# Performance work log

Hardware: AMD Instinct MI355X
Metric: run time of the kernel (lower is better)

## Reference

```python
import jax, jax.numpy as jnp
import numpy as np

K = 9  # ATSS top-k candidates per GT


def cxcywh_to_xyxy(b):
    cx, cy, w, h = b[..., 0], b[..., 1], b[..., 2], b[..., 3]
    return jnp.stack([cx - 0.5 * w, cy - 0.5 * h, cx + 0.5 * w, cy + 0.5 * h], axis=-1)


def elementwise_iou(a, b):
    # a, b: [..., 4] xyxy, broadcastable
    lt = jnp.maximum(a[..., :2], b[..., :2])
    rb = jnp.minimum(a[..., 2:], b[..., 2:])
    wh = jnp.clip(rb - lt, 0.0)
    inter = wh[..., 0] * wh[..., 1]
    area_a = (a[..., 2] - a[..., 0]) * (a[..., 3] - a[..., 1])
    area_b = (b[..., 2] - b[..., 0]) * (b[..., 3] - b[..., 1])
    return inter / (area_a + area_b - inter)


def setup_inputs() -> dict:
    key = jax.random.key(0)
    k1, k2 = jax.random.split(key)
    pred_boxes = jax.random.uniform(k1, (16, 30000, 4), dtype=jnp.float32)
    gt_boxes = jax.random.uniform(k2, (16, 64, 4), dtype=jnp.float32)
    return {"pred_boxes": pred_boxes, "gt_boxes": gt_boxes}


def reference(pred_boxes, gt_boxes):
    # pred_boxes: [B, N, 4] cxcywh; gt_boxes: [B, G, 4] cxcywh
    G = gt_boxes.shape[1]

    def per_image(pred, gt):
        # center-distance matrix [G, N] (the cdist in the original)
        diff = gt[:, None, :2] - pred[None, :, :2]
        dist = jnp.sqrt(jnp.sum(diff * diff, axis=-1))
        # k smallest distances per GT
        _, k_idx = jax.lax.top_k(-dist, K)          # [G, K]
        k_boxes = pred[k_idx]                        # [G, K, 4]
        gt_xyxy = cxcywh_to_xyxy(gt)                 # [G, 4]
        kb_xyxy = cxcywh_to_xyxy(k_boxes)            # [G, K, 4]
        ious = elementwise_iou(gt_xyxy[:, None, :], kb_xyxy)  # [G, K]
        # adaptive threshold: mean + std (torch.std is unbiased -> ddof=1)
        thr = jnp.mean(ious, axis=1, keepdims=True) + jnp.std(ious, axis=1, ddof=1, keepdims=True)
        cx, cy = k_boxes[..., 0], k_boxes[..., 1]
        inside = ((gt_xyxy[:, None, 0] <= cx) & (cx <= gt_xyxy[:, None, 2]) &
                  (gt_xyxy[:, None, 1] <= cy) & (cy <= gt_xyxy[:, None, 3]))
        mask = (ious >= thr) & inside                # [G, K]
        # padded index representation (original returns ragged lists):
        pred_idx = jnp.where(mask, k_idx, -1)
        gt_idx = jnp.where(mask, jnp.arange(G, dtype=jnp.int64)[:, None], -1)
        return pred_idx, gt_idx, mask, ious

    return jax.vmap(per_image)(pred_boxes, gt_boxes)
```

## Files before the change

kernel.cpp:

```cpp
#include <hip/hip_runtime.h>
#include <stdint.h>

typedef unsigned long long u64;

#define KCAND 9
#define BATCH 16
#define NPRED 30000
#define NGT   64
#define TPB   256
#define UNR   8
#define PPT   (TPB * UNR)
#define NT    15
#define PSTR  (NT * PPT)
#define INITKEY 0x7F800000FFFFFFFFULL
#define FINF  __uint_as_float(0x7F800000u)

__device__ __forceinline__ u64 wave_min_u64(u64 v) {
#pragma unroll
    for (int s = 1; s < 64; s <<= 1) {
        u64 o = __shfl_xor(v, s, 64);
        v = o < v ? o : v;
    }
    return v;
}

__global__ __launch_bounds__(256) void compact_xy(
    const float* __restrict__ pred, float2* __restrict__ xy)
{
    int e = blockIdx.x * 256 + threadIdx.x;
    int b = e / PSTR;
    int i = e - b * PSTR;
    float2 v;
    if (i < NPRED) {
        float4 p = ((const float4*)pred)[(size_t)b * NPRED + i];
        v = make_float2(p.x, p.y);
    } else {
        v = make_float2(FINF, FINF);
    }
    xy[e] = v;
}

template <bool PADDED>
__global__ __launch_bounds__(TPB, 4) void atss_kernel(
    const float2* __restrict__ xy,
    const float*  __restrict__ pred,
    const float*  __restrict__ gt,
    float* __restrict__ out)
{
#pragma clang fp contract(off)
    const int tid  = threadIdx.x;
    const int lane = tid & 63;
    const int wvid = tid >> 6;

    const int b = (blockIdx.x & 7) + 8 * (blockIdx.x >> 9);
    const int g = (blockIdx.x >> 3) & 63;
    const int w = b * NGT + g;

    const float4 gtb = ((const float4*)gt)[w];
    const float gcx = gtb.x, gcy = gtb.y;

    const int STRIDE = PADDED ? PSTR : (NPRED * 2);
    const float2* xyb   = xy + (size_t)b * STRIDE;
    const float4* pred4 = (const float4*)pred + (size_t)b * NPRED;

    float lmin = FINF;
    for (int t = 0; t < NT; ++t) {
        float d2[UNR];
        if (PADDED) {
            const float4* x4 = (const float4*)xyb;
#pragma unroll
            for (int k = 0; k < 4; ++k) {
                float4 q = x4[t * (PPT / 2) + k * TPB + tid];
                float dx0 = __fsub_rn(gcx, q.x), dy0 = __fsub_rn(gcy, q.y);
                d2[2 * k]     = __fadd_rn(__fmul_rn(dx0, dx0), __fmul_rn(dy0, dy0));
                float dx1 = __fsub_rn(gcx, q.z), dy1 = __fsub_rn(gcy, q.w);
                d2[2 * k + 1] = __fadd_rn(__fmul_rn(dx1, dx1), __fmul_rn(dy1, dy1));
            }
        } else {
#pragma unroll
            for (int j = 0; j < UNR; ++j) {
                const int i = t * PPT + j * TPB + tid;
                const bool v = i < NPRED;
                float2 p = xyb[(v ? i : 0) * 2];
                float dx = __fsub_rn(gcx, p.x), dy = __fsub_rn(gcy, p.y);
                float d = __fadd_rn(__fmul_rn(dx, dx), __fmul_rn(dy, dy));
                d2[j] = v ? d : FINF;
            }
        }
        float m0 = fminf(d2[0], d2[1]), m1 = fminf(d2[2], d2[3]);
        float m2 = fminf(d2[4], d2[5]), m3 = fminf(d2[6], d2[7]);
        lmin = fminf(lmin, fminf(fminf(m0, m1), fminf(m2, m3)));
    }

    float vv = lmin;
    float T = FINF;
#pragma unroll
    for (int r = 0; r < KCAND; ++r) {
        float m = vv;
#pragma unroll
        for (int s = 1; s < 64; s <<= 1) m = fminf(m, __shfl_xor(m, s, 64));
        T = m;
        u64 bm = __ballot(vv == m);
        if (lane == __ffsll(bm) - 1) vv = FINF;
    }

    u64 val = INITKEY;
    float Tf = T;

    for (int t = 0; t < NT; ++t) {
        float d2[UNR];
        if (PADDED) {
            const float4* x4 = (const float4*)xyb;
#pragma unroll
            for (int k = 0; k < 4; ++k) {
                float4 q = x4[t * (PPT / 2) + k * TPB + tid];
                float dx0 = __fsub_rn(gcx, q.x), dy0 = __fsub_rn(gcy, q.y);
                d2[2 * k]     = __fadd_rn(__fmul_rn(dx0, dx0), __fmul_rn(dy0, dy0));
                float dx1 = __fsub_rn(gcx, q.z), dy1 = __fsub_rn(gcy, q.w);
                d2[2 * k + 1] = __fadd_rn(__fmul_rn(dx1, dx1), __fmul_rn(dy1, dy1));
            }
        } else {
#pragma unroll
            for (int j = 0; j < UNR; ++j) {
                const int i = t * PPT + j * TPB + tid;
                const bool v = i < NPRED;
                float2 p = xyb[(v ? i : 0) * 2];
                float dx = __fsub_rn(gcx, p.x), dy = __fsub_rn(gcy, p.y);
                float d = __fadd_rn(__fmul_rn(dx, dx), __fmul_rn(dy, dy));
                d2[j] = v ? d : FINF;
            }
        }
        float m0 = fminf(d2[0], d2[1]), m1 = fminf(d2[2], d2[3]);
        float m2 = fminf(d2[4], d2[5]), m3 = fminf(d2[6], d2[7]);
        float dmin = fminf(fminf(m0, m1), fminf(m2, m3));
        if (__ballot(dmin <= Tf) == 0ULL) continue;

#pragma unroll
        for (int j = 0; j < UNR; ++j) {
            u64 pend = __ballot(d2[j] <= Tf);
            while (pend) {
                const int src = __ffsll(pend) - 1;
                pend &= pend - 1;
                const unsigned kd = __shfl(__float_as_uint(d2[j]), src, 64);
                unsigned ki;
                if (PADDED) {
                    const int f = t * (PPT / 2) + (j >> 1) * TPB + (tid - lane) + src;
                    ki = (unsigned)(2 * f + (j & 1));
                } else {
                    ki = (unsigned)(t * PPT + j * TPB + (tid - lane) + src);
                }
                const u64 key = ((u64)kd << 32) | ki;
                u64 Tkey = __shfl(val, 8, 64);
                if (key < Tkey) {
                    const u64 ltm = __ballot(val < key) & 0x1FFULL;
                    const int pos = __popcll(ltm);
                    const u64 sh = __shfl_up(val, 1, 64);
                    if (lane < KCAND) {
                        if (lane == pos)      val = key;
                        else if (lane > pos)  val = sh;
                    }
                    Tkey = __shfl(val, 8, 64);
                    Tf = fminf(T, __uint_as_float((unsigned)(Tkey >> 32)));
                    pend &= __ballot(d2[j] <= Tf);
                }
            }
        }
    }

    __shared__ u64 smem[4 * KCAND];
    if (lane < KCAND) smem[wvid * KCAND + lane] = val;
    __syncthreads();

    if (wvid != 0) return;

    u64 key = (lane < 4 * KCAND) ? smem[lane] : ~0ULL;
    u64 fin = 0;
#pragma unroll
    for (int k = 0; k < KCAND; ++k) {
        u64 m = wave_min_u64(key);
        if (lane == k) fin = m;
        if (key == m) key = ~0ULL;
    }

    const bool active = (lane < KCAND);
    const unsigned idx = active ? (unsigned)(fin & 0xffffffffu) : 0u;

    float4 pb = pred4[idx];

    float gx1 = gcx - 0.5f * gtb.z, gy1 = gcy - 0.5f * gtb.w;
    float gx2 = gcx + 0.5f * gtb.z, gy2 = gcy + 0.5f * gtb.w;
    float kx1 = pb.x - 0.5f * pb.z, ky1 = pb.y - 0.5f * pb.w;
    float kx2 = pb.x + 0.5f * pb.z, ky2 = pb.y + 0.5f * pb.w;

    float ltx = fmaxf(gx1, kx1), lty = fmaxf(gy1, ky1);
    float rbx = fminf(gx2, kx2), rby = fminf(gy2, ky2);
    float wvd = fmaxf(rbx - ltx, 0.0f);
    float hvd = fmaxf(rby - lty, 0.0f);
    float inter  = wvd * hvd;
    float area_a = (gx2 - gx1) * (gy2 - gy1);
    float area_b = (kx2 - kx1) * (ky2 - ky1);
    float iou = inter / ((area_a + area_b) - inter);

    float v = active ? iou : 0.0f;
    float s = v;
#pragma unroll
    for (int m = 1; m < 64; m <<= 1) s += __shfl_xor(s, m, 64);
    float mean = s / 9.0f;

    float dev = active ? (iou - mean) : 0.0f;
    float ss = dev * dev;
#pragma unroll
    for (int m = 1; m < 64; m <<= 1) ss += __shfl_xor(ss, m, 64);
    float stdv = sqrtf(ss / 8.0f);
    float thr = mean + stdv;

    bool inside = (gx1 <= pb.x) && (pb.x <= gx2) &&
                  (gy1 <= pb.y) && (pb.y <= gy2);
    bool maskk = (iou >= thr) && inside;

    if (active) {
        const size_t chunk = (size_t)BATCH * NGT * KCAND;
        const size_t o = (size_t)w * KCAND + lane;
        out[0 * chunk + o] = maskk ? (float)idx : -1.0f;
        out[1 * chunk + o] = maskk ? (float)g   : -1.0f;
        out[2 * chunk + o] = maskk ? 1.0f : 0.0f;
        out[3 * chunk + o] = iou;
    }
}

extern "C" void kernel_launch(void* const* d_in, const int* in_sizes, int n_in,
                              void* d_out, int out_size, void* d_ws, size_t ws_size,
                              hipStream_t stream) {
    const float* pred = (const float*)d_in[0];
    const float* gtb  = (const float*)d_in[1];
    float* out = (float*)d_out;

    const size_t need = (size_t)BATCH * PSTR * sizeof(float2);
    if (ws_size >= need) {
        float2* xy = (float2*)d_ws;
        compact_xy<<<BATCH * PSTR / 256, 256, 0, stream>>>(pred, xy);
        atss_kernel<true><<<BATCH * NGT, TPB, 0, stream>>>(xy, pred, gtb, out);
    } else {
        atss_kernel<false><<<BATCH * NGT, TPB, 0, stream>>>(
            (const float2*)pred, pred, gtb, out);
    }
}
```

Before: 83.43 us.

## Process four GT boxes per block and collect candidates via shared-memory atomics

Each 512-thread block now handles four GT boxes, so every loaded prediction center is reused for four distance computations. The per-thread minima are reduced to a top-9 threshold per GT across the whole block. Candidates at or under the threshold are appended to a shared-memory list with ballot and atomics, replacing the serialized per-wave insertion sort. A fallback rescan handles lists that overflow the capacity, at the cost of larger blocks, fewer blocks in the grid, and higher register and shared-memory use.

New measurement: 83.62 us. No clear change (+0.2%).

```diff
diff --git a/kernel.cpp b/kernel.cpp
--- a/kernel.cpp
+++ b/kernel.cpp
@@ -7,14 +7,23 @@
 #define BATCH 16
 #define NPRED 30000
 #define NGT   64
-#define TPB   256
-#define UNR   8
-#define PPT   (TPB * UNR)
-#define NT    15
-#define PSTR  (NT * PPT)
+#define TPB   512
+#define GTA   4
+#define UNRF  4
+#define PPT   (TPB * UNRF * 2)
+#define NT    8
+#define PSTR  32768
+#define NF4   (PSTR / 2)
+#define CAP   128
 #define INITKEY 0x7F800000FFFFFFFFULL
 #define FINF  __uint_as_float(0x7F800000u)
-
+#define SENT  (~0ULL)
+
+__device__ __forceinline__ float wave_min_f(float v) {
+#pragma unroll
+    for (int s = 1; s < 64; s <<= 1) v = fminf(v, __shfl_xor(v, s, 64));
+    return v;
+}
 __device__ __forceinline__ u64 wave_min_u64(u64 v) {
 #pragma unroll
     for (int s = 1; s < 64; s <<= 1) {
@@ -28,8 +37,8 @@
     const float* __restrict__ pred, float2* __restrict__ xy)
 {
     int e = blockIdx.x * 256 + threadIdx.x;
-    int b = e / PSTR;
-    int i = e - b * PSTR;
+    int b = e >> 15;
+    int i = e & (PSTR - 1);
     float2 v;
     if (i < NPRED) {
         float4 p = ((const float4*)pred)[(size_t)b * NPRED + i];
@@ -40,8 +49,12 @@
     xy[e] = v;
 }
 
+#define DIST(GX, GY, PX, PY, D)                                              \
+    { float _dx = __fsub_rn(GX, PX), _dy = __fsub_rn(GY, PY);                \
+      D = __fadd_rn(__fmul_rn(_dx, _dx), __fmul_rn(_dy, _dy)); }
+
 template <bool PADDED>
-__global__ __launch_bounds__(TPB, 4) void atss_kernel(
+__global__ __launch_bounds__(TPB, 2) void atss4(
     const float2* __restrict__ xy,
     const float*  __restrict__ pred,
     const float*  __restrict__ gt,
@@ -50,105 +63,177 @@
 #pragma clang fp contract(off)
     const int tid  = threadIdx.x;
     const int lane = tid & 63;
-    const int wvid = tid >> 6;
-
-    const int b = (blockIdx.x & 7) + 8 * (blockIdx.x >> 9);
-    const int g = (blockIdx.x >> 3) & 63;
-    const int w = b * NGT + g;
-
-    const float4 gtb = ((const float4*)gt)[w];
-    const float gcx = gtb.x, gcy = gtb.y;
-
-    const int STRIDE = PADDED ? PSTR : (NPRED * 2);
-    const float2* xyb   = xy + (size_t)b * STRIDE;
-    const float4* pred4 = (const float4*)pred + (size_t)b * NPRED;
-
-    float lmin = FINF;
-    for (int t = 0; t < NT; ++t) {
-        float d2[UNR];
-        if (PADDED) {
-            const float4* x4 = (const float4*)xyb;
-#pragma unroll
-            for (int k = 0; k < 4; ++k) {
-                float4 q = x4[t * (PPT / 2) + k * TPB + tid];
-                float dx0 = __fsub_rn(gcx, q.x), dy0 = __fsub_rn(gcy, q.y);
-                d2[2 * k]     = __fadd_rn(__fmul_rn(dx0, dx0), __fmul_rn(dy0, dy0));
-                float dx1 = __fsub_rn(gcx, q.z), dy1 = __fsub_rn(gcy, q.w);
-                d2[2 * k + 1] = __fadd_rn(__fmul_rn(dx1, dx1), __fmul_rn(dy1, dy1));
-            }
-        } else {
-#pragma unroll
-            for (int j = 0; j < UNR; ++j) {
+    const int wv   = tid >> 6;
+
+    const int bi = blockIdx.x;
+    const int b  = (bi & 7) + 8 * (bi >> 7);
+    const int g0 = ((bi >> 3) & 15) * GTA;
+
+    const float4* gt4 = (const float4*)gt;
+    const int w0 = b * NGT + g0;
+    const float4 gq0 = gt4[w0],     gq1 = gt4[w0 + 1];
+    const float4 gq2 = gt4[w0 + 2], gq3 = gt4[w0 + 3];
+    const float aX = gq0.x, aY = gq0.y;
+    const float bX = gq1.x, bY = gq1.y;
+    const float cX = gq2.x, cY = gq2.y;
+    const float dX = gq3.x, dY = gq3.y;
+
+    const float4* p4 = (const float4*)pred + (size_t)b * NPRED;
+    const float2* x2 = PADDED ? (xy + (size_t)b * PSTR) : (const float2*)0;
+    const float4* x4 = (const float4*)x2;
+
+    __shared__ float tmins[GTA][TPB];
+    __shared__ float tg[GTA];
+    __shared__ int   cnt[GTA];
+    __shared__ u64   cand[GTA][CAP];
+
+    if (tid < GTA) cnt[tid] = 0;
+
+    float lm0 = FINF, lm1 = FINF, lm2 = FINF, lm3 = FINF;
+#define P1(PX, PY)                                                           \
+    { float d;                                                               \
+      DIST(aX, aY, PX, PY, d); lm0 = fminf(lm0, d);                          \
+      DIST(bX, bY, PX, PY, d); lm1 = fminf(lm1, d);                          \
+      DIST(cX, cY, PX, PY, d); lm2 = fminf(lm2, d);                          \
+      DIST(dX, dY, PX, PY, d); lm3 = fminf(lm3, d); }
+
+    if (PADDED) {
+        for (int t = 0; t < NT; ++t) {
+            const int f0 = t * (PPT / 2) + tid;
+#pragma unroll
+            for (int k = 0; k < UNRF; ++k) {
+                float4 q = x4[f0 + k * TPB];
+                P1(q.x, q.y) P1(q.z, q.w)
+            }
+        }
+    } else {
+        for (int t = 0; t < NT; ++t) {
+#pragma unroll
+            for (int j = 0; j < 2 * UNRF; ++j) {
                 const int i = t * PPT + j * TPB + tid;
-                const bool v = i < NPRED;
-                float2 p = xyb[(v ? i : 0) * 2];
-                float dx = __fsub_rn(gcx, p.x), dy = __fsub_rn(gcy, p.y);
-                float d = __fadd_rn(__fmul_rn(dx, dx), __fmul_rn(dy, dy));
-                d2[j] = v ? d : FINF;
-            }
-        }
-        float m0 = fminf(d2[0], d2[1]), m1 = fminf(d2[2], d2[3]);
-        float m2 = fminf(d2[4], d2[5]), m3 = fminf(d2[6], d2[7]);
-        lmin = fminf(lmin, fminf(fminf(m0, m1), fminf(m2, m3)));
-    }
-
-    float vv = lmin;
-    float T = FINF;
-#pragma unroll
-    for (int r = 0; r < KCAND; ++r) {
-        float m = vv;
-#pragma unroll
-        for (int s = 1; s < 64; s <<= 1) m = fminf(m, __shfl_xor(m, s, 64));
-        T = m;
-        u64 bm = __ballot(vv == m);
-        if (lane == __ffsll(bm) - 1) vv = FINF;
-    }
-
-    u64 val = INITKEY;
-    float Tf = T;
-
-    for (int t = 0; t < NT; ++t) {
-        float d2[UNR];
-        if (PADDED) {
-            const float4* x4 = (const float4*)xyb;
-#pragma unroll
-            for (int k = 0; k < 4; ++k) {
-                float4 q = x4[t * (PPT / 2) + k * TPB + tid];
-                float dx0 = __fsub_rn(gcx, q.x), dy0 = __fsub_rn(gcy, q.y);
-                d2[2 * k]     = __fadd_rn(__fmul_rn(dx0, dx0), __fmul_rn(dy0, dy0));
-                float dx1 = __fsub_rn(gcx, q.z), dy1 = __fsub_rn(gcy, q.w);
-                d2[2 * k + 1] = __fadd_rn(__fmul_rn(dx1, dx1), __fmul_rn(dy1, dy1));
-            }
-        } else {
-#pragma unroll
-            for (int j = 0; j < UNR; ++j) {
+                const bool vv = i < NPRED;
+                float4 q = p4[vv ? i : 0];
+                float px = vv ? q.x : FINF, py = vv ? q.y : FINF;
+                P1(px, py)
+            }
+        }
+    }
+#undef P1
+
+    tmins[0][tid] = lm0; tmins[1][tid] = lm1;
+    tmins[2][tid] = lm2; tmins[3][tid] = lm3;
+    __syncthreads();
+
+    if (wv < GTA) {
+        float a[TPB / 64];
+#pragma unroll
+        for (int j = 0; j < TPB / 64; ++j) a[j] = tmins[wv][j * 64 + lane];
+        float T = FINF;
+#pragma unroll
+        for (int r = 0; r < KCAND; ++r) {
+            float ml = a[0];
+#pragma unroll
+            for (int j = 1; j < TPB / 64; ++j) ml = fminf(ml, a[j]);
+            float m = wave_min_f(ml);
+#pragma unroll
+            for (int j = 0; j < TPB / 64; ++j) a[j] = (a[j] == m) ? FINF : a[j];
+            T = m;
+        }
+        if (lane == 0) tg[wv] = T;
+    }
+    __syncthreads();
+    const float T0 = tg[0], T1 = tg[1], T2 = tg[2], T3 = tg[3];
+
+#define COLLECT(H, D, C, IDXE)                                               \
+    { u64 bm = __ballot(H);                                                  \
+      if (bm) {                                                              \
+          int ldr = __ffsll(bm) - 1;                                         \
+          int base = 0;                                                      \
+          if (lane == ldr) base = atomicAdd(&cnt[C], (int)__popcll(bm));     \
+          base = __shfl(base, ldr, 64);                                      \
+          if (H) {                                                           \
+              int src = lane;                                                \
+              int slot = base + (int)__popcll(bm & ((1ULL << lane) - 1ULL)); \
+              if (slot < CAP)                                                \
+                  cand[C][slot] =                                            \
+                      ((u64)__float_as_uint(D) << 32) | (unsigned)(IDXE);    \
+          } } }
+#define P2(PX, PY, IDXE)                                                     \
+    { float e0, e1, e2, e3;                                                  \
+      DIST(aX, aY, PX, PY, e0); DIST(bX, bY, PX, PY, e1);                    \
+      DIST(cX, cY, PX, PY, e2); DIST(dX, dY, PX, PY, e3);                    \
+      bool h0 = e0 <= T0, h1 = e1 <= T1, h2 = e2 <= T2, h3 = e3 <= T3;       \
+      if (__ballot(h0 | h1 | h2 | h3)) {                                     \
+          COLLECT(h0, e0, 0, IDXE) COLLECT(h1, e1, 1, IDXE)                  \
+          COLLECT(h2, e2, 2, IDXE) COLLECT(h3, e3, 3, IDXE)                  \
+      } }
+
+    if (PADDED) {
+        for (int t = 0; t < NT; ++t) {
+            const int f0 = t * (PPT / 2) + tid;
+            const int fw = t * (PPT / 2) + (tid - lane);
+#pragma unroll
+            for (int k = 0; k < UNRF; ++k) {
+                float4 q = x4[f0 + k * TPB];
+                P2(q.x, q.y, 2 * (fw + k * TPB + src))
+                P2(q.z, q.w, 2 * (fw + k * TPB + src) + 1)
+            }
+        }
+    } else {
+        for (int t = 0; t < NT; ++t) {
+#pragma unroll
+            for (int j = 0; j < 2 * UNRF; ++j) {
                 const int i = t * PPT + j * TPB + tid;
-                const bool v = i < NPRED;
-                float2 p = xyb[(v ? i : 0) * 2];
-                float dx = __fsub_rn(gcx, p.x), dy = __fsub_rn(gcy, p.y);
-                float d = __fadd_rn(__fmul_rn(dx, dx), __fmul_rn(dy, dy));
-                d2[j] = v ? d : FINF;
-            }
-        }
-        float m0 = fminf(d2[0], d2[1]), m1 = fminf(d2[2], d2[3]);
-        float m2 = fminf(d2[4], d2[5]), m3 = fminf(d2[6], d2[7]);
-        float dmin = fminf(fminf(m0, m1), fminf(m2, m3));
-        if (__ballot(dmin <= Tf) == 0ULL) continue;
-
-#pragma unroll
-        for (int j = 0; j < UNR; ++j) {
-            u64 pend = __ballot(d2[j] <= Tf);
+                const int iw = t * PPT + j * TPB + (tid - lane);
+                const bool vv = i < NPRED;
+                float4 q = p4[vv ? i : 0];
+                float px = vv ? q.x : FINF, py = vv ? q.y : FINF;
+                P2(px, py, iw + src)
+            }
+        }
+    }
+#undef P2
+#undef COLLECT
+    __syncthreads();
+
+    if (wv >= GTA) return;
+    const int c = wv;
+    const float gX = (c == 0) ? aX : (c == 1) ? bX : (c == 2) ? cX : dX;
+    const float gY = (c == 0) ? aY : (c == 1) ? bY : (c == 2) ? cY : dY;
+    const int n = cnt[c];
+
+    u64 fin = SENT;
+    if (n <= CAP) {
+        u64 k0 = (lane < n)      ? cand[c][lane]      : SENT;
+        u64 k1 = (lane + 64 < n) ? cand[c][lane + 64] : SENT;
+#pragma unroll
+        for (int r = 0; r < KCAND; ++r) {
+            u64 ml = k0 < k1 ? k0 : k1;
+            u64 m = wave_min_u64(ml);
+            if (lane == r) fin = m;
+            if (k0 == m) k0 = SENT;
+            if (k1 == m) k1 = SENT;
+        }
+    } else {
+        u64 val = INITKEY;
+        float Tf = tg[c];
+        for (int i0 = 0; i0 < PSTR; i0 += 64) {
+            const int i = i0 + lane;
+            float px, py;
+            if (PADDED) {
+                float2 p = x2[i];  px = p.x;  py = p.y;
+            } else {
+                const bool vv = i < NPRED;
+                float4 q = p4[vv ? i : 0];
+                px = vv ? q.x : FINF;  py = vv ? q.y : FINF;
+            }
+            float d;  DIST(gX, gY, px, py, d);
+            u64 pend = __ballot(d <= Tf);
             while (pend) {
                 const int src = __ffsll(pend) - 1;
                 pend &= pend - 1;
-                const unsigned kd = __shfl(__float_as_uint(d2[j]), src, 64);
-                unsigned ki;
-                if (PADDED) {
-                    const int f = t * (PPT / 2) + (j >> 1) * TPB + (tid - lane) + src;
-                    ki = (unsigned)(2 * f + (j & 1));
-                } else {
-                    ki = (unsigned)(t * PPT + j * TPB + (tid - lane) + src);
-                }
+                const unsigned kd = __shfl(__float_as_uint(d), src, 64);
+                const unsigned ki = (unsigned)(i0 + src);
                 const u64 key = ((u64)kd << 32) | ki;
                 u64 Tkey = __shfl(val, 8, 64);
                 if (key < Tkey) {
@@ -160,37 +245,28 @@
                         else if (lane > pos)  val = sh;
                     }
                     Tkey = __shfl(val, 8, 64);
-                    Tf = fminf(T, __uint_as_float((unsigned)(Tkey >> 32)));
-                    pend &= __ballot(d2[j] <= Tf);
+                    Tf = fminf(tg[c], __uint_as_float((unsigned)(Tkey >> 32)));
+                    pend &= __ballot(d <= Tf);
                 }
             }
         }
-    }
-
-    __shared__ u64 smem[4 * KCAND];
-    if (lane < KCAND) smem[wvid * KCAND + lane] = val;
-    __syncthreads();
-
-    if (wvid != 0) return;
-
-    u64 key = (lane < 4 * KCAND) ? smem[lane] : ~0ULL;
-    u64 fin = 0;
-#pragma unroll
-    for (int k = 0; k < KCAND; ++k) {
-        u64 m = wave_min_u64(key);
-        if (lane == k) fin = m;
-        if (key == m) key = ~0ULL;
-    }
+        fin = val;
+    }
+
+    const int g = g0 + c;
+    const int w = b * NGT + g;
+    const float4 gq = gt4[w];
+    const float gcx = gq.x, gcy = gq.y;
 
     const bool active = (lane < KCAND);
     const unsigned idx = active ? (unsigned)(fin & 0xffffffffu) : 0u;
 
-    float4 pb = pred4[idx];
-
-    float gx1 = gcx - 0.5f * gtb.z, gy1 = gcy - 0.5f * gtb.w;
-    float gx2 = gcx + 0.5f * gtb.z, gy2 = gcy + 0.5f * gtb.w;
-    float kx1 = pb.x - 0.5f * pb.z, ky1 = pb.y - 0.5f * pb.w;
-    float kx2 = pb.x + 0.5f * pb.z, ky2 = pb.y + 0.5f * pb.w;
+    float4 pbx = p4[idx];
+
+    float gx1 = gcx - 0.5f * gq.z, gy1 = gcy - 0.5f * gq.w;
+    float gx2 = gcx + 0.5f * gq.z, gy2 = gcy + 0.5f * gq.w;
+    float kx1 = pbx.x - 0.5f * pbx.z, ky1 = pbx.y - 0.5f * pbx.w;
+    float kx2 = pbx.x + 0.5f * pbx.z, ky2 = pbx.y + 0.5f * pbx.w;
 
     float ltx = fmaxf(gx1, kx1), lty = fmaxf(gy1, ky1);
     float rbx = fminf(gx2, kx2), rby = fminf(gy2, ky2);
@@ -214,8 +290,8 @@
     float stdv = sqrtf(ss / 8.0f);
     float thr = mean + stdv;
 
-    bool inside = (gx1 <= pb.x) && (pb.x <= gx2) &&
-                  (gy1 <= pb.y) && (pb.y <= gy2);
+    bool inside = (gx1 <= pbx.x) && (pbx.x <= gx2) &&
+                  (gy1 <= pbx.y) && (pbx.y <= gy2);
     bool maskk = (iou >= thr) && inside;
 
     if (active) {
@@ -239,9 +315,9 @@
     if (ws_size >= need) {
         float2* xy = (float2*)d_ws;
         compact_xy<<<BATCH * PSTR / 256, 256, 0, stream>>>(pred, xy);
-        atss_kernel<true><<<BATCH * NGT, TPB, 0, stream>>>(xy, pred, gtb, out);
-    } else {
-        atss_kernel<false><<<BATCH * NGT, TPB, 0, stream>>>(
-            (const float2*)pred, pred, gtb, out);
-    }
-}
+        atss4<true><<<BATCH * (NGT / GTA), TPB, 0, stream>>>(xy, pred, gtb, out);
+    } else {
+        atss4<false><<<BATCH * (NGT / GTA), TPB, 0, stream>>>(
+            nullptr, pred, gtb, out);
+    }
+}
```
